# Kernel optimization log

Hardware: AMD Instinct MI355X
Metric: run time of the kernel (lower is better)

Reference implementation:

```python
import jax, jax.numpy as jnp
import numpy as np

R_TBR = 0.5
P_BASE = 50.0
ALPHA = 100.0
H_BASELINE = 0.0
T_AMBIENT = -10.0
EPS = 1e-8


def _ternary_quantize(weight):
    gamma = jnp.mean(jnp.abs(weight))
    # round-half-to-even matches torch.round
    return jnp.clip(jnp.round(weight / (gamma + EPS)), -1.0, 1.0)


def _entropy_3bin(w_q):
    n = w_q.size
    # histc(bins=3, min=-1, max=1) on values in {-1,0,1} -> exact bin counts
    counts = jnp.stack([
        jnp.sum(w_q == -1.0),
        jnp.sum(w_q == 0.0),
        jnp.sum(w_q == 1.0),
    ]).astype(jnp.float32)
    p = counts / n
    # -sum p*log2 p over p>0 (jnp.where keeps it jit-safe)
    return -jnp.sum(jnp.where(p > 0, p * jnp.log2(jnp.where(p > 0, p, 1.0)), 0.0))


def setup_inputs() -> dict:
    key = jax.random.key(0)
    k1, k2 = jax.random.split(key)
    x = jax.random.normal(k1, (8192, 4096), dtype=jnp.float32)
    weight = jax.random.normal(k2, (4096, 4096), dtype=jnp.float32)  # [out, in]
    return {"x": x, "weight": weight}


def reference(x, weight):
    w_q = _ternary_quantize(weight)            # ternary {-1,0,1}, shape [out, in]
    entropy = _entropy_3bin(w_q)
    heat_flux = ALPHA * jax.nn.relu(entropy - H_BASELINE)
    q_total = P_BASE + heat_flux
    t_current = T_AMBIENT + q_total * R_TBR    # guardrail value (no overload at T_ambient=-10)
    output = x @ w_q.T                         # F.linear(x, W_q), [N, out]
    return (output, t_current, entropy)
```

## Files before the change

### kernel.cpp

```cpp
#include <hip/hip_runtime.h>
#include <stdint.h>

typedef short bf16x8 __attribute__((ext_vector_type(8)));
typedef float f32x4 __attribute__((ext_vector_type(4)));

#define M_ROWS 8192
#define N_OUT  4096
#define K_DIM  4096
#define NW     16777216.0

__device__ __forceinline__ void gload16(const void* g, void* l) {
    __builtin_amdgcn_global_load_lds((const __attribute__((address_space(1))) void*)g,
                                     (__attribute__((address_space(3))) void*)l,
                                     16, 0, 0);
}

__device__ __forceinline__ unsigned short f2bf(float f) {
    unsigned u = __float_as_uint(f);
    unsigned r = 0x7FFFu + ((u >> 16) & 1u);
    return (unsigned short)((u + r) >> 16);
}

__global__ __launch_bounds__(256) void k_gamma(const float* __restrict__ w,
                                               double* __restrict__ sum) {
    const int n4 = (K_DIM * N_OUT) / 4;
    int idx = blockIdx.x * blockDim.x + threadIdx.x;
    int stride = gridDim.x * blockDim.x;
    const float4* w4 = (const float4*)w;
    double local = 0.0;
    for (int i = idx; i < n4; i += stride) {
        float4 v = w4[i];
        local += (double)fabsf(v.x) + (double)fabsf(v.y) +
                 (double)fabsf(v.z) + (double)fabsf(v.w);
    }
    __shared__ double sm[256];
    sm[threadIdx.x] = local;
    __syncthreads();
    for (int s = 128; s > 0; s >>= 1) {
        if (threadIdx.x < s) sm[threadIdx.x] += sm[threadIdx.x + s];
        __syncthreads();
    }
    if (threadIdx.x == 0) atomicAdd(sum, sm[0]);
}

__global__ __launch_bounds__(256) void k_quant(const float* __restrict__ w,
                                               const double* __restrict__ sum,
                                               unsigned short* __restrict__ wq,
                                               unsigned int* __restrict__ counts,
                                               int do_store) {
    const float gamma = (float)(*sum / NW);
    const float denom = gamma + 1e-8f;
    const int n4 = (K_DIM * N_OUT) / 4;
    int idx = blockIdx.x * blockDim.x + threadIdx.x;
    int stride = gridDim.x * blockDim.x;
    const float4* w4 = (const float4*)w;
    unsigned cm = 0, cp = 0;
    for (int i = idx; i < n4; i += stride) {
        float4 v = w4[i];
        float q0 = fminf(1.f, fmaxf(-1.f, rintf(v.x / denom)));
        float q1 = fminf(1.f, fmaxf(-1.f, rintf(v.y / denom)));
        float q2 = fminf(1.f, fmaxf(-1.f, rintf(v.z / denom)));
        float q3 = fminf(1.f, fmaxf(-1.f, rintf(v.w / denom)));
        cm += (q0 < -0.5f) + (q1 < -0.5f) + (q2 < -0.5f) + (q3 < -0.5f);
        cp += (q0 >  0.5f) + (q1 >  0.5f) + (q2 >  0.5f) + (q3 >  0.5f);
        if (do_store) {
            unsigned b0 = (q0 < -0.5f) ? 0xBF80u : (q0 > 0.5f ? 0x3F80u : 0u);
            unsigned b1 = (q1 < -0.5f) ? 0xBF80u : (q1 > 0.5f ? 0x3F80u : 0u);
            unsigned b2 = (q2 < -0.5f) ? 0xBF80u : (q2 > 0.5f ? 0x3F80u : 0u);
            unsigned b3 = (q3 < -0.5f) ? 0xBF80u : (q3 > 0.5f ? 0x3F80u : 0u);
            uint2 pk;
            pk.x = b0 | (b1 << 16);
            pk.y = b2 | (b3 << 16);
            ((uint2*)wq)[i] = pk;
        }
    }
    __shared__ unsigned smc[512];
    smc[threadIdx.x] = cm;
    smc[256 + threadIdx.x] = cp;
    __syncthreads();
    for (int s = 128; s > 0; s >>= 1) {
        if (threadIdx.x < s) {
            smc[threadIdx.x] += smc[threadIdx.x + s];
            smc[256 + threadIdx.x] += smc[256 + threadIdx.x + s];
        }
        __syncthreads();
    }
    if (threadIdx.x == 0) {
        atomicAdd(&counts[0], smc[0]);
        atomicAdd(&counts[1], smc[256]);
    }
}

__global__ __launch_bounds__(256) void k_cvt(const float* __restrict__ x,
                                             unsigned short* __restrict__ xb) {
    const int n4 = (M_ROWS * K_DIM) / 4;
    int idx = blockIdx.x * blockDim.x + threadIdx.x;
    int stride = gridDim.x * blockDim.x;
    const float4* x4 = (const float4*)x;
    for (int i = idx; i < n4; i += stride) {
        float4 v = x4[i];
        uint2 pk;
        pk.x = (unsigned)f2bf(v.x) | ((unsigned)f2bf(v.y) << 16);
        pk.y = (unsigned)f2bf(v.z) | ((unsigned)f2bf(v.w) << 16);
        ((uint2*)xb)[i] = pk;
    }
}

__global__ void k_fin(const unsigned int* __restrict__ counts,
                      float* __restrict__ outs) {
    double n = NW;
    double c1 = (double)counts[0];
    double c2 = (double)counts[1];
    double c0 = n - c1 - c2;
    double H = 0.0;
    if (c1 > 0.0) { double p = c1 / n; H -= p * log2(p); }
    if (c0 > 0.0) { double p = c0 / n; H -= p * log2(p); }
    if (c2 > 0.0) { double p = c2 / n; H -= p * log2(p); }
    float Hf = (float)H;
    float heat = 100.0f * fmaxf(Hf, 0.0f);
    outs[0] = -10.0f + (50.0f + heat) * 0.5f;
    outs[1] = Hf;
}


__device__ __forceinline__ void stage_half(const unsigned short* __restrict__ A,
                                           const unsigned short* __restrict__ B,
                                           char* lds, int H, int tm, int tn,
                                           int tid) {
    const int kt = H >> 2;
    const int q  = H & 3;
    const unsigned short* src = (q & 2) ? B : A;
    const int rb = ((q & 2) ? tn : tm) * 256 + (q & 1) * 128;
    const int row = rb + ((tid >> 6) << 4) + (tid & 15);
    const unsigned short* g0 = src + (size_t)row * K_DIM + kt * 64 + ((tid >> 4) & 3) * 8;
    char* d = lds + ((size_t)(kt & 1) << 16) + (q << 14) + tid * 16;
    gload16(g0, d);
    gload16(g0 + 32, d + 8192);
}

#define MFMA_Q(ACCM, ACCN, AF, BF)                                             \
    __builtin_amdgcn_s_setprio(1);                                             \
    _Pragma("unroll") for (int mm = 0; mm < 4; ++mm)                           \
    _Pragma("unroll") for (int nn = 0; nn < 2; ++nn)                           \
    _Pragma("unroll") for (int ks = 0; ks < 2; ++ks)                           \
        acc[(ACCM) + mm][(ACCN) + nn] = __builtin_amdgcn_mfma_f32_16x16x32_bf16( \
            AF[mm][ks], BF[nn][ks], acc[(ACCM) + mm][(ACCN) + nn], 0, 0, 0);   \
    __builtin_amdgcn_s_setprio(0);

__global__ __launch_bounds__(512, 2) void k_gemm2(const unsigned short* __restrict__ A,
                                                  const unsigned short* __restrict__ B,
                                                  float* __restrict__ C) {
    extern __shared__ char smem[];
    const int tid  = threadIdx.x;
    const int lane = tid & 63;
    const int wid  = tid >> 6;
    const int wr   = wid >> 2;
    const int wc   = wid & 3;
    const int fr   = lane & 15;
    const int khi  = lane >> 4;

    const int lin = blockIdx.x;
    const int s   = (lin & 7) * 64 + (lin >> 3);
    const int tm  = s & 31;
    const int tn  = s >> 5;

    f32x4 acc[8][4] = {};

    stage_half(A, B, smem, 0, tm, tn, tid);
    stage_half(A, B, smem, 1, tm, tn, tid);
    stage_half(A, B, smem, 2, tm, tn, tid);
    stage_half(A, B, smem, 3, tm, tn, tid);
    stage_half(A, B, smem, 6, tm, tn, tid);
    stage_half(A, B, smem, 7, tm, tn, tid);
    asm volatile("s_waitcnt vmcnt(0)" ::: "memory");

    bf16x8 afr[4][2], b0[2][2], b1[2][2];
    const int bsel = (wc & 1) * 4;

    for (int tau = 0; tau < 64; ++tau) {
        const char* aptr = smem + ((size_t)(tau & 1) << 16) + ((size_t)wr << 14) + lane * 16;
        const char* bptr = smem + ((size_t)(tau & 1) << 16) + 32768 + ((size_t)(wc >> 1) << 14)
                         + bsel * 1024 + lane * 16;
        const int g = tau * 4;

        __builtin_amdgcn_s_barrier();
        __builtin_amdgcn_sched_barrier(0);

#pragma unroll
        for (int mm = 0; mm < 4; ++mm)
#pragma unroll
            for (int ks = 0; ks < 2; ++ks)
                afr[mm][ks] = *(const bf16x8*)(aptr + (ks * 8 + mm) * 1024);
#pragma unroll
        for (int nn = 0; nn < 2; ++nn)
#pragma unroll
            for (int ks = 0; ks < 2; ++ks)
                b0[nn][ks] = *(const bf16x8*)(bptr + (ks * 8 + nn) * 1024);
        if (g + 4 < 256) stage_half(A, B, smem, g + 4, tm, tn, tid);
        MFMA_Q(0, 0, afr, b0)

#pragma unroll
        for (int nn = 0; nn < 2; ++nn)
#pragma unroll
            for (int ks = 0; ks < 2; ++ks)
                b1[nn][ks] = *(const bf16x8*)(bptr + (ks * 8 + 2 + nn) * 1024);
        if (g + 5 < 256) stage_half(A, B, smem, g + 5, tm, tn, tid);
        MFMA_Q(0, 2, afr, b1)

#pragma unroll
        for (int mm = 0; mm < 4; ++mm)
#pragma unroll
            for (int ks = 0; ks < 2; ++ks)
                afr[mm][ks] = *(const bf16x8*)(aptr + (ks * 8 + 4 + mm) * 1024);
        MFMA_Q(4, 2, afr, b1)
        MFMA_Q(4, 0, afr, b0)

        __builtin_amdgcn_sched_barrier(0);
        __builtin_amdgcn_s_barrier();
        __builtin_amdgcn_sched_barrier(0);

        if (g + 10 < 256) stage_half(A, B, smem, g + 10, tm, tn, tid);
        if (g + 11 < 256) stage_half(A, B, smem, g + 11, tm, tn, tid);
        if (tau < 62) {
            asm volatile("s_waitcnt vmcnt(4)" ::: "memory");
        } else {
            asm volatile("s_waitcnt vmcnt(0)" ::: "memory");
        }
    }

    const size_t crow = (size_t)(tm * 256 + wr * 128 + khi * 4);
    const int    ccol = tn * 256 + wc * 64 + fr;
#pragma unroll
    for (int m = 0; m < 8; ++m)
#pragma unroll
        for (int n = 0; n < 4; ++n) {
            float* cp = C + (crow + m * 16) * N_OUT + (ccol + n * 16);
#pragma unroll
            for (int j = 0; j < 4; ++j)
                cp[(size_t)j * N_OUT] = acc[m][n][j];
        }
}

__global__ __launch_bounds__(256) void fb_gemm(const float* __restrict__ X,
                                               const float* __restrict__ W,
                                               const double* __restrict__ sum,
                                               float* __restrict__ C) {
    __shared__ float Xs[64][33];
    __shared__ float Ws[64][33];
    const float gamma = (float)(*sum / NW);
    const float denom = gamma + 1e-8f;
    const int tid = threadIdx.x;
    const int bm = blockIdx.y * 64;
    const int bn = blockIdx.x * 64;
    const int tr = tid >> 4, tc = tid & 15;
    const int lrow = tid >> 2;
    const int lcol = (tid & 3) * 8;
    float acc[4][4] = {};
    for (int k0 = 0; k0 < K_DIM; k0 += 32) {
        const float4* xs = (const float4*)(X + (size_t)(bm + lrow) * K_DIM + k0 + lcol);
        float4 v0 = xs[0], v1 = xs[1];
        Xs[lrow][lcol + 0] = v0.x; Xs[lrow][lcol + 1] = v0.y;
        Xs[lrow][lcol + 2] = v0.z; Xs[lrow][lcol + 3] = v0.w;
        Xs[lrow][lcol + 4] = v1.x; Xs[lrow][lcol + 5] = v1.y;
        Xs[lrow][lcol + 6] = v1.z; Xs[lrow][lcol + 7] = v1.w;
        const float4* wsrc = (const float4*)(W + (size_t)(bn + lrow) * K_DIM + k0 + lcol);
        float4 w0 = wsrc[0], w1 = wsrc[1];
        Ws[lrow][lcol + 0] = fminf(1.f, fmaxf(-1.f, rintf(w0.x / denom)));
        Ws[lrow][lcol + 1] = fminf(1.f, fmaxf(-1.f, rintf(w0.y / denom)));
        Ws[lrow][lcol + 2] = fminf(1.f, fmaxf(-1.f, rintf(w0.z / denom)));
        Ws[lrow][lcol + 3] = fminf(1.f, fmaxf(-1.f, rintf(w0.w / denom)));
        Ws[lrow][lcol + 4] = fminf(1.f, fmaxf(-1.f, rintf(w1.x / denom)));
        Ws[lrow][lcol + 5] = fminf(1.f, fmaxf(-1.f, rintf(w1.y / denom)));
        Ws[lrow][lcol + 6] = fminf(1.f, fmaxf(-1.f, rintf(w1.z / denom)));
        Ws[lrow][lcol + 7] = fminf(1.f, fmaxf(-1.f, rintf(w1.w / denom)));
        __syncthreads();
#pragma unroll 8
        for (int kk = 0; kk < 32; ++kk) {
            float a0 = Xs[tr * 4 + 0][kk], a1 = Xs[tr * 4 + 1][kk];
            float a2 = Xs[tr * 4 + 2][kk], a3 = Xs[tr * 4 + 3][kk];
            float b0 = Ws[tc * 4 + 0][kk], b1 = Ws[tc * 4 + 1][kk];
            float b2 = Ws[tc * 4 + 2][kk], b3 = Ws[tc * 4 + 3][kk];
            acc[0][0] += a0 * b0; acc[0][1] += a0 * b1; acc[0][2] += a0 * b2; acc[0][3] += a0 * b3;
            acc[1][0] += a1 * b0; acc[1][1] += a1 * b1; acc[1][2] += a1 * b2; acc[1][3] += a1 * b3;
            acc[2][0] += a2 * b0; acc[2][1] += a2 * b1; acc[2][2] += a2 * b2; acc[2][3] += a2 * b3;
            acc[3][0] += a3 * b0; acc[3][1] += a3 * b1; acc[3][2] += a3 * b2; acc[3][3] += a3 * b3;
        }
        __syncthreads();
    }
#pragma unroll
    for (int i = 0; i < 4; ++i)
#pragma unroll
        for (int j = 0; j < 4; ++j)
            C[(size_t)(bm + tr * 4 + i) * N_OUT + (bn + tc * 4 + j)] = acc[i][j];
}

extern "C" void kernel_launch(void* const* d_in, const int* in_sizes, int n_in,
                              void* d_out, int out_size, void* d_ws, size_t ws_size,
                              hipStream_t stream) {
    (void)in_sizes; (void)n_in; (void)out_size;
    const float* x = (const float*)d_in[0];
    const float* w = (const float*)d_in[1];
    float* out = (float*)d_out;
    float* scalars = out + (size_t)M_ROWS * N_OUT;

    double* sum = (double*)d_ws;
    unsigned int* counts = (unsigned int*)((char*)d_ws + 8);
    unsigned short* xb = (unsigned short*)((char*)d_ws + 64);
    unsigned short* wq = (unsigned short*)((char*)d_ws + 64 + (size_t)M_ROWS * K_DIM * 2);

    const size_t need = 64 + (size_t)M_ROWS * K_DIM * 2 + (size_t)N_OUT * K_DIM * 2;
    const int fast = (ws_size >= need);

    hipMemsetAsync(d_ws, 0, 16, stream);
    k_gamma<<<1024, 256, 0, stream>>>(w, sum);

    if (fast) {
        k_cvt<<<2048, 256, 0, stream>>>(x, xb);
        k_quant<<<1024, 256, 0, stream>>>(w, sum, wq, counts, 1);
        k_fin<<<1, 1, 0, stream>>>(counts, scalars);
        hipFuncSetAttribute(reinterpret_cast<const void*>(k_gemm2),
                            hipFuncAttributeMaxDynamicSharedMemorySize, 131072);
        k_gemm2<<<dim3(512), 512, 131072, stream>>>(xb, wq, out);
    } else {
        k_quant<<<1024, 256, 0, stream>>>(w, sum, nullptr, counts, 0);
        k_fin<<<1, 1, 0, stream>>>(counts, scalars);
        dim3 grid(N_OUT / 64, M_ROWS / 64);
        fb_gemm<<<grid, 256, 0, stream>>>(x, w, sum, out);
    }
}
```

Baseline: 377.6 us.

## Unroll GEMM main loop over both LDS buffers with ping-pong barriers and remap tiles

Rewrites the bf16 MFMA GEMM main loop to unroll two K-steps per iteration with fixed even/odd LDS pointers. Each MFMA quarter is now bracketed by workgroup barriers and an explicit lgkmcnt wait, so the waves move in lockstep, alternating LDS reads and global prefetch with compute. The block-to-tile mapping also changes to group tiles into 16x4 regions per XCD slot, aiming for better L2 reuse. The extra barriers per step add synchronisation overhead and could stall the waves if the interleaving does not balance.

New measurement: 367.9 us. -2.6%, faster.

```diff
diff --git a/kernel.cpp b/kernel.cpp
--- a/kernel.cpp
+++ b/kernel.cpp
@@ -147,6 +147,19 @@
             AF[mm][ks], BF[nn][ks], acc[(ACCM) + mm][(ACCN) + nn], 0, 0, 0);   \
     __builtin_amdgcn_s_setprio(0);
 
+#define RD_A(PTR, BASE)                                                        \
+    _Pragma("unroll") for (int mm = 0; mm < 4; ++mm)                           \
+    _Pragma("unroll") for (int ks = 0; ks < 2; ++ks)                           \
+        afr[mm][ks] = *(const bf16x8*)((PTR) + (ks * 8 + (BASE) + mm) * 1024);
+
+#define RD_B(PTR, BASE, DST)                                                   \
+    _Pragma("unroll") for (int nn = 0; nn < 2; ++nn)                           \
+    _Pragma("unroll") for (int ks = 0; ks < 2; ++ks)                           \
+        DST[nn][ks] = *(const bf16x8*)((PTR) + (ks * 8 + (BASE) + nn) * 1024);
+
+#define BAR  __builtin_amdgcn_s_barrier()
+#define LGKM0 asm volatile("s_waitcnt lgkmcnt(0)" ::: "memory")
+
 __global__ __launch_bounds__(512, 2) void k_gemm2(const unsigned short* __restrict__ A,
                                                   const unsigned short* __restrict__ B,
                                                   float* __restrict__ C) {
@@ -160,9 +173,10 @@
     const int khi  = lane >> 4;
 
     const int lin = blockIdx.x;
-    const int s   = (lin & 7) * 64 + (lin >> 3);
-    const int tm  = s & 31;
-    const int tn  = s >> 5;
+    const int x   = lin & 7;
+    const int j   = lin >> 3;
+    const int tm  = ((x & 1) << 4) + (j & 15);
+    const int tn  = ((x >> 1) << 2) + (j >> 4);
 
     f32x4 acc[8][4] = {};
 
@@ -172,61 +186,74 @@
     stage_half(A, B, smem, 3, tm, tn, tid);
     stage_half(A, B, smem, 6, tm, tn, tid);
     stage_half(A, B, smem, 7, tm, tn, tid);
-    asm volatile("s_waitcnt vmcnt(0)" ::: "memory");
+    asm volatile("s_waitcnt vmcnt(4)" ::: "memory");
+    BAR;
 
     bf16x8 afr[4][2], b0[2][2], b1[2][2];
     const int bsel = (wc & 1) * 4;
 
-    for (int tau = 0; tau < 64; ++tau) {
-        const char* aptr = smem + ((size_t)(tau & 1) << 16) + ((size_t)wr << 14) + lane * 16;
-        const char* bptr = smem + ((size_t)(tau & 1) << 16) + 32768 + ((size_t)(wc >> 1) << 14)
-                         + bsel * 1024 + lane * 16;
-        const int g = tau * 4;
-
-        __builtin_amdgcn_s_barrier();
-        __builtin_amdgcn_sched_barrier(0);
-
-#pragma unroll
-        for (int mm = 0; mm < 4; ++mm)
-#pragma unroll
-            for (int ks = 0; ks < 2; ++ks)
-                afr[mm][ks] = *(const bf16x8*)(aptr + (ks * 8 + mm) * 1024);
-#pragma unroll
-        for (int nn = 0; nn < 2; ++nn)
-#pragma unroll
-            for (int ks = 0; ks < 2; ++ks)
-                b0[nn][ks] = *(const bf16x8*)(bptr + (ks * 8 + nn) * 1024);
-        if (g + 4 < 256) stage_half(A, B, smem, g + 4, tm, tn, tid);
+    const char* aE = smem + ((size_t)wr << 14) + lane * 16;
+    const char* bE = smem + 32768 + ((size_t)(wc >> 1) << 14) + bsel * 1024 + lane * 16;
+    const char* aO = aE + 65536;
+    const char* bO = bE + 65536;
+
+    for (int it = 0; it < 32; ++it) {
+        const int g = it * 8;
+        const bool more = (it < 31);
+
+        RD_A(aE, 0)
+        RD_B(bE, 0, b0)
+        stage_half(A, B, smem, g + 4, tm, tn, tid);
+        BAR; LGKM0;
         MFMA_Q(0, 0, afr, b0)
-
-#pragma unroll
-        for (int nn = 0; nn < 2; ++nn)
-#pragma unroll
-            for (int ks = 0; ks < 2; ++ks)
-                b1[nn][ks] = *(const bf16x8*)(bptr + (ks * 8 + 2 + nn) * 1024);
-        if (g + 5 < 256) stage_half(A, B, smem, g + 5, tm, tn, tid);
+        BAR;
+
+        RD_B(bE, 2, b1)
+        stage_half(A, B, smem, g + 5, tm, tn, tid);
+        BAR; LGKM0;
         MFMA_Q(0, 2, afr, b1)
-
-#pragma unroll
-        for (int mm = 0; mm < 4; ++mm)
-#pragma unroll
-            for (int ks = 0; ks < 2; ++ks)
-                afr[mm][ks] = *(const bf16x8*)(aptr + (ks * 8 + 4 + mm) * 1024);
+        BAR;
+
+        RD_A(aE, 4)
+        if (more) stage_half(A, B, smem, g + 10, tm, tn, tid);
+        BAR; LGKM0;
         MFMA_Q(4, 2, afr, b1)
+        BAR;
+
+        if (more) stage_half(A, B, smem, g + 11, tm, tn, tid);
+        BAR; LGKM0;
         MFMA_Q(4, 0, afr, b0)
-
-        __builtin_amdgcn_sched_barrier(0);
-        __builtin_amdgcn_s_barrier();
-        __builtin_amdgcn_sched_barrier(0);
-
-        if (g + 10 < 256) stage_half(A, B, smem, g + 10, tm, tn, tid);
-        if (g + 11 < 256) stage_half(A, B, smem, g + 11, tm, tn, tid);
-        if (tau < 62) {
-            asm volatile("s_waitcnt vmcnt(4)" ::: "memory");
-        } else {
-            asm volatile("s_waitcnt vmcnt(0)" ::: "memory");
-        }
-    }
+        if (more) { asm volatile("s_waitcnt vmcnt(4)" ::: "memory"); }
+        else      { asm volatile("s_waitcnt vmcnt(0)" ::: "memory"); }
+        BAR;
+
+        RD_A(aO, 0)
+        RD_B(bO, 0, b0)
+        if (more) stage_half(A, B, smem, g + 8, tm, tn, tid);
+        BAR; LGKM0;
+        MFMA_Q(0, 0, afr, b0)
+        BAR;
+
+        RD_B(bO, 2, b1)
+        if (more) stage_half(A, B, smem, g + 9, tm, tn, tid);
+        BAR; LGKM0;
+        MFMA_Q(0, 2, afr, b1)
+        BAR;
+
+        RD_A(aO, 4)
+        if (more) stage_half(A, B, smem, g + 14, tm, tn, tid);
+        BAR; LGKM0;
+        MFMA_Q(4, 2, afr, b1)
+        BAR;
+
+        if (more) stage_half(A, B, smem, g + 15, tm, tn, tid);
+        BAR; LGKM0;
+        MFMA_Q(4, 0, afr, b0)
+        if (more) { asm volatile("s_waitcnt vmcnt(4)" ::: "memory"); }
+        else      { asm volatile("s_waitcnt vmcnt(0)" ::: "memory"); }
+        BAR;
+    }
+    asm volatile("s_waitcnt vmcnt(0)" ::: "memory");
 
     const size_t crow = (size_t)(tm * 256 + wr * 128 + khi * 4);
     const int    ccol = tn * 256 + wc * 64 + fr;
@@ -236,8 +263,8 @@
         for (int n = 0; n < 4; ++n) {
             float* cp = C + (crow + m * 16) * N_OUT + (ccol + n * 16);
 #pragma unroll
-            for (int j = 0; j < 4; ++j)
-                cp[(size_t)j * N_OUT] = acc[m][n][j];
+            for (int jj = 0; jj < 4; ++jj)
+                cp[(size_t)jj * N_OUT] = acc[m][n][jj];
         }
 }
 
@@ -290,8 +317,8 @@
 #pragma unroll
     for (int i = 0; i < 4; ++i)
 #pragma unroll
-        for (int j = 0; j < 4; ++j)
-            C[(size_t)(bm + tr * 4 + i) * N_OUT + (bn + tc * 4 + j)] = acc[i][j];
+        for (int jj = 0; jj < 4; ++jj)
+            C[(size_t)(bm + tr * 4 + i) * N_OUT + (bn + tc * 4 + jj)] = acc[i][jj];
 }
 
 extern "C" void kernel_launch(void* const* d_in, const int* in_sizes, int n_in,
```
